# Optimization experiments

Hardware: AMD Instinct MI355X
Metric: run time of the kernel (lower is better)

Reference implementation:

```python
import jax, jax.numpy as jnp
import numpy as np

ALPHA = 2.0
INF = 1e12  # stand-in for +inf, safe in fp32 arithmetic here


def _sq_dt_last(f):
    """Generalized 1D squared distance transform along the last axis.
    D[..., p] = min_q (p - q)^2 + f[..., q]  (Felzenszwalb DT, brute-force min)."""
    n = f.shape[-1]
    i = jnp.arange(n, dtype=f.dtype)
    cost = (i[:, None] - i[None, :]) ** 2  # [q, p]
    # [..., q, 1] + [q, p] -> min over q
    return jnp.min(f[..., :, None] + cost, axis=-2)


def _edt(mask):
    """Exact 2D Euclidean distance transform: distance from each True pixel
    to the nearest False pixel (0 at False pixels), matching scipy's
    distance_transform_edt(mask). mask: bool [B, H, W]."""
    f = jnp.where(mask, jnp.float32(INF), jnp.float32(0.0))
    # pass along H (axis 1)
    f = jnp.moveaxis(_sq_dt_last(jnp.moveaxis(f, 1, -1)), -1, 1)
    # pass along W (axis 2)
    f = _sq_dt_last(f)
    return jnp.sqrt(f)


def _distance_field(img):
    """fg_dist + bg_dist per batch element; zero field if no foreground
    (mirrors the fg_mask.any() check in the torch code)."""
    fg = img > 0.5
    field = _edt(fg) + _edt(~fg)
    has_fg = jnp.any(fg, axis=(1, 2), keepdims=True)
    return jnp.where(has_fg, field, jnp.float32(0.0))


def setup_inputs() -> dict:
    key = jax.random.key(0)
    k1, k2 = jax.random.split(key)
    pred = jax.random.normal(k1, (8, 192, 192), dtype=jnp.float32)   # logits
    target = jax.random.uniform(k2, (8, 192, 192), dtype=jnp.float32)
    return {"pred": pred, "target": target}


def reference(pred, target):
    p = jax.nn.sigmoid(pred)
    # distance fields are computed via numpy/scipy in the original -> constants
    pred_dt = jax.lax.stop_gradient(_distance_field(p))
    target_dt = jax.lax.stop_gradient(_distance_field(target))
    pred_error = (p - target) ** 2
    distance = (pred_dt ** ALPHA + target_dt ** ALPHA) / (pred_dt + target_dt) ** ALPHA
    dt_field = pred_error * distance
    loss = jnp.mean(dt_field, axis=-1)
    return jnp.mean(loss)
```

## Files before the change

kernel.cpp:

```cpp
#include <hip/hip_runtime.h>
#include <stdint.h>

#define B 8
#define H 192
#define W 192
#define NPIX (B * H * W)
#define NROWS (B * H)
#define NCOL (B * W)
#define INFF 1e12f

__device__ __forceinline__ int hi_pos(uint64_t w0, uint64_t w1, uint64_t w2) {
  if (w2) return 191 - __builtin_clzll(w2);
  if (w1) return 127 - __builtin_clzll(w1);
  if (w0) return 63 - __builtin_clzll(w0);
  return -255;
}
__device__ __forceinline__ int lo_pos(uint64_t w0, uint64_t w1, uint64_t w2) {
  if (w0) return __builtin_ctzll(w0);
  if (w1) return 64 + __builtin_ctzll(w1);
  if (w2) return 128 + __builtin_ctzll(w2);
  return 447;
}
__device__ __forceinline__ int nearest_dist(uint64_t s0, uint64_t s1,
                                            uint64_t s2, int h) {
  int k = h >> 6, r = h & 63;
  uint64_t keepL = (2ull << r) - 1;
  uint64_t b0 = s0, b1 = s1, b2 = s2;
  if (k == 0) { b0 &= keepL; b1 = 0; b2 = 0; }
  else if (k == 1) { b1 &= keepL; b2 = 0; }
  else { b2 &= keepL; }
  int dbelow = h - hi_pos(b0, b1, b2);
  uint64_t keepU = (~0ull) << r;
  uint64_t a0 = s0, a1 = s1, a2 = s2;
  if (k == 0) { a0 &= keepU; }
  else if (k == 1) { a0 = 0; a1 &= keepU; }
  else { a0 = 0; a1 = 0; a2 &= keepU; }
  int dabove = lo_pos(a0, a1, a2) - h;
  return min(min(dbelow, dabove), 255);
}

__global__ __launch_bounds__(192) void col_mask(
    const float* __restrict__ pred, const float* __restrict__ targ,
    uint64_t* __restrict__ masks) {
  int bw = blockIdx.x;
  int b = bw / W, w = bw % W;
  int h = threadIdx.x;
  int idx = b * H * W + h * W + w;
  uint64_t bp = __ballot(pred[idx] > 0.0f);
  uint64_t bt = __ballot(targ[idx] > 0.5f);
  if ((h & 63) == 0) {
    int wv = h >> 6;
    masks[wv * NCOL + bw] = bp;
    masks[(3 + wv) * NCOL + bw] = bt;
  }
}

__global__ __launch_bounds__(192) void row_pass(
    const float* __restrict__ pred, const float* __restrict__ targ,
    const uint64_t* __restrict__ masks, float* __restrict__ partial) {
  int bh = blockIdx.x;
  int b = bh / H, h = bh % H;
  int w = threadIdx.x;
  __shared__ uint32_t sm[W];
  __shared__ float wsum[3];
  int cw = b * W + w;
  uint64_t p0 = masks[0 * NCOL + cw], p1 = masks[1 * NCOL + cw],
           p2 = masks[2 * NCOL + cw];
  uint64_t q0 = masks[3 * NCOL + cw], q1 = masks[4 * NCOL + cw],
           q2 = masks[5 * NCOL + cw];
  int base = b * H * W + h * W;
  float xv = pred[base + w];
  float tv = targ[base + w];

  int k = h >> 6, rb = h & 63;
  uint64_t pw = (k == 0) ? p0 : ((k == 1) ? p1 : p2);
  uint64_t qw = (k == 0) ? q0 : ((k == 1) ? q1 : q2);
  int mp = (int)((pw >> rb) & 1);
  int mt = (int)((qw >> rb) & 1);
  int sp = nearest_dist(mp ? ~p0 : p0, mp ? ~p1 : p1, mp ? ~p2 : p2, h);
  int st = nearest_dist(mt ? ~q0 : q0, mt ? ~q1 : q1, mt ? ~q2 : q2, h);
  int dFp = mp ? sp : 0, dTp = mp ? 0 : sp;
  int dFt = mt ? st : 0, dTt = mt ? 0 : st;
  uint32_t own = (uint32_t)dFp | ((uint32_t)dTp << 8) | ((uint32_t)dFt << 16) |
                 ((uint32_t)dTt << 24);
  sm[w] = own;
  __syncthreads();

  int shp = (xv > 0.0f) ? 0 : 8;
  int sht = (tv > 0.5f) ? 16 : 24;
  int dp = (own >> shp) & 255;
  int dt = (own >> sht) & 255;
  float bp = (dp == 255) ? INFF : (float)(dp * dp);
  float bt = (dt == 255) ? INFF : (float)(dt * dt);
  for (int r = 1; r < W; ++r) {
    float rr = (float)(r * r);
    if (rr >= fmaxf(bp, bt)) break;
    int ql = w - r, qr = w + r;
    if (ql >= 0) {
      uint32_t v = sm[ql];
      int a = (v >> shp) & 255, c = (v >> sht) & 255;
      bp = fminf(bp, (a == 255) ? INFF : rr + (float)(a * a));
      bt = fminf(bt, (c == 255) ? INFF : rr + (float)(c * c));
    }
    if (qr < W) {
      uint32_t v = sm[qr];
      int a = (v >> shp) & 255, c = (v >> sht) & 255;
      bp = fminf(bp, (a == 255) ? INFF : rr + (float)(a * a));
      bt = fminf(bt, (c == 255) ? INFF : rr + (float)(c * c));
    }
  }

  float p = 1.0f / (1.0f + __expf(-xv));
  float e = p - tv;
  float err = e * e;
  float pd = sqrtf(bp), td = sqrtf(bt);
  float s = pd + td;
  float term = err * (bp + bt) / (s * s);

  for (int off = 32; off > 0; off >>= 1) term += __shfl_down(term, off, 64);
  if ((w & 63) == 0) wsum[w >> 6] = term;
  __syncthreads();
  if (w == 0) partial[bh] = wsum[0] + wsum[1] + wsum[2];
}

__global__ __launch_bounds__(256) void reduce_pass(
    const float* __restrict__ partial, float* __restrict__ out) {
  int t = threadIdx.x;
  float s = 0.0f;
#pragma unroll
  for (int i = t; i < NROWS; i += 256) s += partial[i];
  for (int off = 32; off > 0; off >>= 1) s += __shfl_down(s, off, 64);
  __shared__ float ws[4];
  if ((t & 63) == 0) ws[t >> 6] = s;
  __syncthreads();
  if (t == 0) out[0] = (ws[0] + ws[1] + ws[2] + ws[3]) * (1.0f / (float)NPIX);
}

extern "C" void kernel_launch(void* const* d_in, const int* in_sizes, int n_in,
                              void* d_out, int out_size, void* d_ws, size_t ws_size,
                              hipStream_t stream) {
  const float* pred = (const float*)d_in[0];
  const float* targ = (const float*)d_in[1];
  float* out = (float*)d_out;
  uint64_t* masks = (uint64_t*)d_ws;
  float* partial = (float*)((char*)d_ws + (size_t)6 * NCOL * 8);

  col_mask<<<NCOL, 192, 0, stream>>>(pred, targ, masks);
  row_pass<<<NROWS, 192, 0, stream>>>(pred, targ, masks, partial);
  reduce_pass<<<1, 256, 0, stream>>>(partial, out);
}
```

Before: 64.87 us.

## Fuse column-mask and row-pass kernels into one block-per-row-group kernel

Merges the column bitmask kernel and the row EDT kernel into one launch. Each block handles one image and a group of 24 rows. The block first builds the column bitmasks for the whole image in shared memory, then processes its rows four at a time with 768 threads. This removes a kernel launch and the global round trip of the masks. In exchange, each of the 8 blocks per image recomputes the full-image masks, which means redundant strided global reads. Only 64 blocks are launched, so occupancy is low.

```diff
diff --git a/kernel.cpp b/kernel.cpp
--- a/kernel.cpp
+++ b/kernel.cpp
@@ -6,8 +6,12 @@
 #define W 192
 #define NPIX (B * H * W)
 #define NROWS (B * H)
-#define NCOL (B * W)
 #define INFF 1e12f
+
+#define SPLITS 8
+#define RPB (H / SPLITS)
+#define SLOTS 4
+#define ITERS (RPB / SLOTS)
 
 __device__ __forceinline__ int hi_pos(uint64_t w0, uint64_t w1, uint64_t w2) {
   if (w2) return 191 - __builtin_clzll(w2);
@@ -39,88 +43,95 @@
   return min(min(dbelow, dabove), 255);
 }
 
-__global__ __launch_bounds__(192) void col_mask(
+__global__ __launch_bounds__(768) void fused_pass(
     const float* __restrict__ pred, const float* __restrict__ targ,
-    uint64_t* __restrict__ masks) {
-  int bw = blockIdx.x;
-  int b = bw / W, w = bw % W;
-  int h = threadIdx.x;
-  int idx = b * H * W + h * W + w;
-  uint64_t bp = __ballot(pred[idx] > 0.0f);
-  uint64_t bt = __ballot(targ[idx] > 0.5f);
-  if ((h & 63) == 0) {
-    int wv = h >> 6;
-    masks[wv * NCOL + bw] = bp;
-    masks[(3 + wv) * NCOL + bw] = bt;
+    float* __restrict__ partial) {
+  int blk = blockIdx.x;
+  int b = blk >> 3, rg = blk & 7;
+  int row0 = rg * RPB;
+  int t = threadIdx.x;
+
+  __shared__ uint64_t cm[2][3][W];
+  __shared__ uint32_t sm[SLOTS][W];
+  __shared__ float wsum[SLOTS][3];
+
+  if (t < 3 * W) {
+    int k = t / W, w = t - k * W;
+    const float* pb = pred + b * H * W;
+    const float* tb = targ + b * H * W;
+    int base = (k << 6) * W + w;
+    uint64_t pw = 0, qw = 0;
+#pragma unroll 16
+    for (int j = 0; j < 64; ++j) {
+      pw |= (uint64_t)(pb[base + j * W] > 0.0f) << j;
+      qw |= (uint64_t)(tb[base + j * W] > 0.5f) << j;
+    }
+    cm[0][k][w] = pw;
+    cm[1][k][w] = qw;
   }
-}
-
-__global__ __launch_bounds__(192) void row_pass(
-    const float* __restrict__ pred, const float* __restrict__ targ,
-    const uint64_t* __restrict__ masks, float* __restrict__ partial) {
-  int bh = blockIdx.x;
-  int b = bh / H, h = bh % H;
-  int w = threadIdx.x;
-  __shared__ uint32_t sm[W];
-  __shared__ float wsum[3];
-  int cw = b * W + w;
-  uint64_t p0 = masks[0 * NCOL + cw], p1 = masks[1 * NCOL + cw],
-           p2 = masks[2 * NCOL + cw];
-  uint64_t q0 = masks[3 * NCOL + cw], q1 = masks[4 * NCOL + cw],
-           q2 = masks[5 * NCOL + cw];
-  int base = b * H * W + h * W;
-  float xv = pred[base + w];
-  float tv = targ[base + w];
-
-  int k = h >> 6, rb = h & 63;
-  uint64_t pw = (k == 0) ? p0 : ((k == 1) ? p1 : p2);
-  uint64_t qw = (k == 0) ? q0 : ((k == 1) ? q1 : q2);
-  int mp = (int)((pw >> rb) & 1);
-  int mt = (int)((qw >> rb) & 1);
-  int sp = nearest_dist(mp ? ~p0 : p0, mp ? ~p1 : p1, mp ? ~p2 : p2, h);
-  int st = nearest_dist(mt ? ~q0 : q0, mt ? ~q1 : q1, mt ? ~q2 : q2, h);
-  int dFp = mp ? sp : 0, dTp = mp ? 0 : sp;
-  int dFt = mt ? st : 0, dTt = mt ? 0 : st;
-  uint32_t own = (uint32_t)dFp | ((uint32_t)dTp << 8) | ((uint32_t)dFt << 16) |
-                 ((uint32_t)dTt << 24);
-  sm[w] = own;
   __syncthreads();
 
-  int shp = (xv > 0.0f) ? 0 : 8;
-  int sht = (tv > 0.5f) ? 16 : 24;
-  int dp = (own >> shp) & 255;
-  int dt = (own >> sht) & 255;
-  float bp = (dp == 255) ? INFF : (float)(dp * dp);
-  float bt = (dt == 255) ? INFF : (float)(dt * dt);
-  for (int r = 1; r < W; ++r) {
-    float rr = (float)(r * r);
-    if (rr >= fmaxf(bp, bt)) break;
-    int ql = w - r, qr = w + r;
-    if (ql >= 0) {
-      uint32_t v = sm[ql];
-      int a = (v >> shp) & 255, c = (v >> sht) & 255;
-      bp = fminf(bp, (a == 255) ? INFF : rr + (float)(a * a));
-      bt = fminf(bt, (c == 255) ? INFF : rr + (float)(c * c));
+  int slot = t / W, w = t - slot * W;
+  uint64_t p0 = cm[0][0][w], p1 = cm[0][1][w], p2 = cm[0][2][w];
+  uint64_t q0 = cm[1][0][w], q1 = cm[1][1][w], q2 = cm[1][2][w];
+
+  for (int it = 0; it < ITERS; ++it) {
+    int h = row0 + it * SLOTS + slot;
+    int base = b * H * W + h * W;
+    float xv = pred[base + w];
+    float tv = targ[base + w];
+
+    int k = h >> 6, rb = h & 63;
+    uint64_t pw = (k == 0) ? p0 : ((k == 1) ? p1 : p2);
+    uint64_t qw = (k == 0) ? q0 : ((k == 1) ? q1 : q2);
+    int mp = (int)((pw >> rb) & 1);
+    int mt = (int)((qw >> rb) & 1);
+    int sp = nearest_dist(mp ? ~p0 : p0, mp ? ~p1 : p1, mp ? ~p2 : p2, h);
+    int st = nearest_dist(mt ? ~q0 : q0, mt ? ~q1 : q1, mt ? ~q2 : q2, h);
+    int dFp = mp ? sp : 0, dTp = mp ? 0 : sp;
+    int dFt = mt ? st : 0, dTt = mt ? 0 : st;
+    uint32_t own = (uint32_t)dFp | ((uint32_t)dTp << 8) |
+                   ((uint32_t)dFt << 16) | ((uint32_t)dTt << 24);
+    sm[slot][w] = own;
+    __syncthreads();
+
+    int shp = (xv > 0.0f) ? 0 : 8;
+    int sht = (tv > 0.5f) ? 16 : 24;
+    int dp = (own >> shp) & 255;
+    int dt = (own >> sht) & 255;
+    float bp = (dp == 255) ? INFF : (float)(dp * dp);
+    float bt = (dt == 255) ? INFF : (float)(dt * dt);
+    for (int r = 1; r < W; ++r) {
+      float rr = (float)(r * r);
+      if (rr >= fmaxf(bp, bt)) break;
+      int ql = w - r, qr = w + r;
+      if (ql >= 0) {
+        uint32_t v = sm[slot][ql];
+        int a = (v >> shp) & 255, c = (v >> sht) & 255;
+        bp = fminf(bp, (a == 255) ? INFF : rr + (float)(a * a));
+        bt = fminf(bt, (c == 255) ? INFF : rr + (float)(c * c));
+      }
+      if (qr < W) {
+        uint32_t v = sm[slot][qr];
+        int a = (v >> shp) & 255, c = (v >> sht) & 255;
+        bp = fminf(bp, (a == 255) ? INFF : rr + (float)(a * a));
+        bt = fminf(bt, (c == 255) ? INFF : rr + (float)(c * c));
+      }
     }
-    if (qr < W) {
-      uint32_t v = sm[qr];
-      int a = (v >> shp) & 255, c = (v >> sht) & 255;
-      bp = fminf(bp, (a == 255) ? INFF : rr + (float)(a * a));
-      bt = fminf(bt, (c == 255) ? INFF : rr + (float)(c * c));
-    }
+
+    float p = 1.0f / (1.0f + __expf(-xv));
+    float e = p - tv;
+    float err = e * e;
+    float pd = sqrtf(bp), td = sqrtf(bt);
+    float s = pd + td;
+    float term = err * (bp + bt) / (s * s);
+
+    for (int off = 32; off > 0; off >>= 1) term += __shfl_down(term, off, 64);
+    if ((w & 63) == 0) wsum[slot][w >> 6] = term;
+    __syncthreads();
+    if (w == 0)
+      partial[b * H + h] = wsum[slot][0] + wsum[slot][1] + wsum[slot][2];
   }
-
-  float p = 1.0f / (1.0f + __expf(-xv));
-  float e = p - tv;
-  float err = e * e;
-  float pd = sqrtf(bp), td = sqrtf(bt);
-  float s = pd + td;
-  float term = err * (bp + bt) / (s * s);
-
-  for (int off = 32; off > 0; off >>= 1) term += __shfl_down(term, off, 64);
-  if ((w & 63) == 0) wsum[w >> 6] = term;
-  __syncthreads();
-  if (w == 0) partial[bh] = wsum[0] + wsum[1] + wsum[2];
 }
 
 __global__ __launch_bounds__(256) void reduce_pass(
@@ -137,15 +148,13 @@
 }
 
 extern "C" void kernel_launch(void* const* d_in, const int* in_sizes, int n_in,
-                              void* d_out, int out_size, void* d_ws, size_t ws_size,
-                              hipStream_t stream) {
+                              void* d_out, int out_size, void* d_ws,
+                              size_t ws_size, hipStream_t stream) {
   const float* pred = (const float*)d_in[0];
   const float* targ = (const float*)d_in[1];
   float* out = (float*)d_out;
-  uint64_t* masks = (uint64_t*)d_ws;
-  float* partial = (float*)((char*)d_ws + (size_t)6 * NCOL * 8);
+  float* partial = (float*)d_ws;
 
-  col_mask<<<NCOL, 192, 0, stream>>>(pred, targ, masks);
-  row_pass<<<NROWS, 192, 0, stream>>>(pred, targ, masks, partial);
+  fused_pass<<<B * SPLITS, 768, 0, stream>>>(pred, targ, partial);
   reduce_pass<<<1, 256, 0, stream>>>(partial, out);
 }
```

Measured after the change: 75.42 us. 1.16x slower.

## Process four rows per block and fold final reduction into atomics

Applied to the files above, without the earlier changes.

The row pass now handles four image rows per block (two slots of 192 threads, two iterations), so each thread loads the six column mask words once and reuses them for several rows. The separate reduction kernel is removed. Each block atomically adds its scaled partial sum into the output, which is zeroed in the column-mask kernel. This drops one kernel launch and reuses mask loads, at the cost of fewer, larger blocks, more barriers per block, and float atomics that make the summation order nondeterministic.

```diff
diff --git a/kernel.cpp b/kernel.cpp
--- a/kernel.cpp
+++ b/kernel.cpp
@@ -8,6 +8,12 @@
 #define NROWS (B * H)
 #define NCOL (B * W)
 #define INFF 1e12f
+
+#define SLOTS 2
+#define ITERS 2
+#define ROWS_PB (SLOTS * ITERS)
+#define NTHR (SLOTS * W)
+#define KBLK (NROWS / ROWS_PB)
 
 __device__ __forceinline__ int hi_pos(uint64_t w0, uint64_t w1, uint64_t w2) {
   if (w2) return 191 - __builtin_clzll(w2);
@@ -41,7 +47,7 @@
 
 __global__ __launch_bounds__(192) void col_mask(
     const float* __restrict__ pred, const float* __restrict__ targ,
-    uint64_t* __restrict__ masks) {
+    uint64_t* __restrict__ masks, float* __restrict__ out) {
   int bw = blockIdx.x;
   int b = bw / W, w = bw % W;
   int h = threadIdx.x;
@@ -53,99 +59,100 @@
     masks[wv * NCOL + bw] = bp;
     masks[(3 + wv) * NCOL + bw] = bt;
   }
+  if (bw == 0 && h == 0) out[0] = 0.0f;
 }
 
-__global__ __launch_bounds__(192) void row_pass(
+__global__ __launch_bounds__(NTHR) void row_pass(
     const float* __restrict__ pred, const float* __restrict__ targ,
-    const uint64_t* __restrict__ masks, float* __restrict__ partial) {
-  int bh = blockIdx.x;
-  int b = bh / H, h = bh % H;
-  int w = threadIdx.x;
-  __shared__ uint32_t sm[W];
-  __shared__ float wsum[3];
+    const uint64_t* __restrict__ masks, float* __restrict__ out) {
+  int blk = blockIdx.x;
+  int bh0 = blk * ROWS_PB;
+  int b = bh0 / H, h0 = bh0 - b * H;
+  int t = threadIdx.x;
+  int slot = t / W, w = t - slot * W;
+
+  __shared__ uint32_t sm[SLOTS][W];
+  __shared__ float wsum[SLOTS][3];
+  __shared__ float rsum[ROWS_PB];
+
   int cw = b * W + w;
   uint64_t p0 = masks[0 * NCOL + cw], p1 = masks[1 * NCOL + cw],
            p2 = masks[2 * NCOL + cw];
   uint64_t q0 = masks[3 * NCOL + cw], q1 = masks[4 * NCOL + cw],
            q2 = masks[5 * NCOL + cw];
-  int base = b * H * W + h * W;
-  float xv = pred[base + w];
-  float tv = targ[base + w];
 
-  int k = h >> 6, rb = h & 63;
-  uint64_t pw = (k == 0) ? p0 : ((k == 1) ? p1 : p2);
-  uint64_t qw = (k == 0) ? q0 : ((k == 1) ? q1 : q2);
-  int mp = (int)((pw >> rb) & 1);
-  int mt = (int)((qw >> rb) & 1);
-  int sp = nearest_dist(mp ? ~p0 : p0, mp ? ~p1 : p1, mp ? ~p2 : p2, h);
-  int st = nearest_dist(mt ? ~q0 : q0, mt ? ~q1 : q1, mt ? ~q2 : q2, h);
-  int dFp = mp ? sp : 0, dTp = mp ? 0 : sp;
-  int dFt = mt ? st : 0, dTt = mt ? 0 : st;
-  uint32_t own = (uint32_t)dFp | ((uint32_t)dTp << 8) | ((uint32_t)dFt << 16) |
-                 ((uint32_t)dTt << 24);
-  sm[w] = own;
+  for (int it = 0; it < ITERS; ++it) {
+    int h = h0 + it * SLOTS + slot;
+    int base = b * H * W + h * W;
+    float xv = pred[base + w];
+    float tv = targ[base + w];
+
+    int k = h >> 6, rb = h & 63;
+    uint64_t pw = (k == 0) ? p0 : ((k == 1) ? p1 : p2);
+    uint64_t qw = (k == 0) ? q0 : ((k == 1) ? q1 : q2);
+    int mp = (int)((pw >> rb) & 1);
+    int mt = (int)((qw >> rb) & 1);
+    int sp = nearest_dist(mp ? ~p0 : p0, mp ? ~p1 : p1, mp ? ~p2 : p2, h);
+    int st = nearest_dist(mt ? ~q0 : q0, mt ? ~q1 : q1, mt ? ~q2 : q2, h);
+    int dFp = mp ? sp : 0, dTp = mp ? 0 : sp;
+    int dFt = mt ? st : 0, dTt = mt ? 0 : st;
+    uint32_t own = (uint32_t)dFp | ((uint32_t)dTp << 8) |
+                   ((uint32_t)dFt << 16) | ((uint32_t)dTt << 24);
+    sm[slot][w] = own;
+    __syncthreads();
+
+    int shp = (xv > 0.0f) ? 0 : 8;
+    int sht = (tv > 0.5f) ? 16 : 24;
+    int dp = (own >> shp) & 255;
+    int dt = (own >> sht) & 255;
+    float bp = (dp == 255) ? INFF : (float)(dp * dp);
+    float bt = (dt == 255) ? INFF : (float)(dt * dt);
+    for (int r = 1; r < W; ++r) {
+      float rr = (float)(r * r);
+      if (rr >= fmaxf(bp, bt)) break;
+      int ql = w - r, qr = w + r;
+      if (ql >= 0) {
+        uint32_t v = sm[slot][ql];
+        int a = (v >> shp) & 255, c = (v >> sht) & 255;
+        bp = fminf(bp, (a == 255) ? INFF : rr + (float)(a * a));
+        bt = fminf(bt, (c == 255) ? INFF : rr + (float)(c * c));
+      }
+      if (qr < W) {
+        uint32_t v = sm[slot][qr];
+        int a = (v >> shp) & 255, c = (v >> sht) & 255;
+        bp = fminf(bp, (a == 255) ? INFF : rr + (float)(a * a));
+        bt = fminf(bt, (c == 255) ? INFF : rr + (float)(c * c));
+      }
+    }
+
+    float p = 1.0f / (1.0f + __expf(-xv));
+    float e = p - tv;
+    float err = e * e;
+    float pd = sqrtf(bp), td = sqrtf(bt);
+    float s = pd + td;
+    float term = err * (bp + bt) / (s * s);
+
+    for (int off = 32; off > 0; off >>= 1) term += __shfl_down(term, off, 64);
+    if ((w & 63) == 0) wsum[slot][w >> 6] = term;
+    __syncthreads();
+    if (w == 0)
+      rsum[it * SLOTS + slot] = wsum[slot][0] + wsum[slot][1] + wsum[slot][2];
+  }
   __syncthreads();
-
-  int shp = (xv > 0.0f) ? 0 : 8;
-  int sht = (tv > 0.5f) ? 16 : 24;
-  int dp = (own >> shp) & 255;
-  int dt = (own >> sht) & 255;
-  float bp = (dp == 255) ? INFF : (float)(dp * dp);
-  float bt = (dt == 255) ? INFF : (float)(dt * dt);
-  for (int r = 1; r < W; ++r) {
-    float rr = (float)(r * r);
-    if (rr >= fmaxf(bp, bt)) break;
-    int ql = w - r, qr = w + r;
-    if (ql >= 0) {
-      uint32_t v = sm[ql];
-      int a = (v >> shp) & 255, c = (v >> sht) & 255;
-      bp = fminf(bp, (a == 255) ? INFF : rr + (float)(a * a));
-      bt = fminf(bt, (c == 255) ? INFF : rr + (float)(c * c));
-    }
-    if (qr < W) {
-      uint32_t v = sm[qr];
-      int a = (v >> shp) & 255, c = (v >> sht) & 255;
-      bp = fminf(bp, (a == 255) ? INFF : rr + (float)(a * a));
-      bt = fminf(bt, (c == 255) ? INFF : rr + (float)(c * c));
-    }
+  if (t == 0) {
+    float bsum = (rsum[0] + rsum[1]) + (rsum[2] + rsum[3]);
+    atomicAdd(out, bsum * (1.0f / (float)NPIX));
   }
-
-  float p = 1.0f / (1.0f + __expf(-xv));
-  float e = p - tv;
-  float err = e * e;
-  float pd = sqrtf(bp), td = sqrtf(bt);
-  float s = pd + td;
-  float term = err * (bp + bt) / (s * s);
-
-  for (int off = 32; off > 0; off >>= 1) term += __shfl_down(term, off, 64);
-  if ((w & 63) == 0) wsum[w >> 6] = term;
-  __syncthreads();
-  if (w == 0) partial[bh] = wsum[0] + wsum[1] + wsum[2];
-}
-
-__global__ __launch_bounds__(256) void reduce_pass(
-    const float* __restrict__ partial, float* __restrict__ out) {
-  int t = threadIdx.x;
-  float s = 0.0f;
-#pragma unroll
-  for (int i = t; i < NROWS; i += 256) s += partial[i];
-  for (int off = 32; off > 0; off >>= 1) s += __shfl_down(s, off, 64);
-  __shared__ float ws[4];
-  if ((t & 63) == 0) ws[t >> 6] = s;
-  __syncthreads();
-  if (t == 0) out[0] = (ws[0] + ws[1] + ws[2] + ws[3]) * (1.0f / (float)NPIX);
 }
 
 extern "C" void kernel_launch(void* const* d_in, const int* in_sizes, int n_in,
-                              void* d_out, int out_size, void* d_ws, size_t ws_size,
-                              hipStream_t stream) {
+                              void* d_out, int out_size, void* d_ws,
+                              size_t ws_size, hipStream_t stream) {
   const float* pred = (const float*)d_in[0];
   const float* targ = (const float*)d_in[1];
   float* out = (float*)d_out;
   uint64_t* masks = (uint64_t*)d_ws;
-  float* partial = (float*)((char*)d_ws + (size_t)6 * NCOL * 8);
 
-  col_mask<<<NCOL, 192, 0, stream>>>(pred, targ, masks);
-  row_pass<<<NROWS, 192, 0, stream>>>(pred, targ, masks, partial);
-  reduce_pass<<<1, 256, 0, stream>>>(partial, out);
+  col_mask<<<NCOL, 192, 0, stream>>>(pred, targ, masks, out);
+  row_pass<<<KBLK, NTHR, 0, stream>>>(pred, targ, masks, out);
 }
```

New measurement: 67.51 us. 4.1% more time.

## Build column bitmasks from coalesced row tiles with shared-memory bit transpose

Applied to the files above, without the earlier changes.

The column-mask kernel used to read one column per block with strided loads (one float per row, stride W). It now loads 64x64 tiles with lanes reading contiguous row segments, ballots each row into a 64-bit row mask in shared memory, then transposes the bits so each thread builds one column word. This replaces poorly coalesced global reads with coalesced ones, at the cost of far fewer blocks (72 versus 1536) and a serial 64-iteration bit-gather loop per output thread.

```diff
diff --git a/kernel.cpp b/kernel.cpp
--- a/kernel.cpp
+++ b/kernel.cpp
@@ -39,19 +39,47 @@
   return min(min(dbelow, dabove), 255);
 }
 
-__global__ __launch_bounds__(192) void col_mask(
+__global__ __launch_bounds__(256) void col_mask(
     const float* __restrict__ pred, const float* __restrict__ targ,
     uint64_t* __restrict__ masks) {
-  int bw = blockIdx.x;
-  int b = bw / W, w = bw % W;
-  int h = threadIdx.x;
-  int idx = b * H * W + h * W + w;
-  uint64_t bp = __ballot(pred[idx] > 0.0f);
-  uint64_t bt = __ballot(targ[idx] > 0.5f);
-  if ((h & 63) == 0) {
-    int wv = h >> 6;
-    masks[wv * NCOL + bw] = bp;
-    masks[(3 + wv) * NCOL + bw] = bt;
+  int blk = blockIdx.x;
+  int b = blk / 9;
+  int rem = blk - b * 9;
+  int wg = rem / 3, k = rem - wg * 3;
+  int t = threadIdx.x;
+  int lane = t & 63, wv = t >> 6;
+
+  __shared__ uint64_t rmp[64];
+  __shared__ uint64_t rmt[64];
+
+  {
+    int j0 = wv * 16;
+    int base = b * H * W + (k * 64 + j0) * W + wg * 64 + lane;
+    float pv[16], tv[16];
+#pragma unroll
+    for (int jj = 0; jj < 16; ++jj) {
+      pv[jj] = pred[base + jj * W];
+      tv[jj] = targ[base + jj * W];
+    }
+#pragma unroll
+    for (int jj = 0; jj < 16; ++jj) {
+      uint64_t bp = __ballot(pv[jj] > 0.0f);
+      uint64_t bt = __ballot(tv[jj] > 0.5f);
+      if (lane == 0) {
+        rmp[j0 + jj] = bp;
+        rmt[j0 + jj] = bt;
+      }
+    }
+  }
+  __syncthreads();
+
+  if (t < 128) {
+    const uint64_t* rm = (t >= 64) ? rmt : rmp;
+    uint64_t wrd = 0;
+#pragma unroll
+    for (int j = 0; j < 64; ++j) wrd |= ((rm[j] >> lane) & 1ull) << j;
+    int word_row = ((t >= 64) ? 3 : 0) + k;
+    masks[word_row * NCOL + b * W + wg * 64 + lane] = wrd;
   }
 }
 
@@ -137,15 +165,15 @@
 }
 
 extern "C" void kernel_launch(void* const* d_in, const int* in_sizes, int n_in,
-                              void* d_out, int out_size, void* d_ws, size_t ws_size,
-                              hipStream_t stream) {
+                              void* d_out, int out_size, void* d_ws,
+                              size_t ws_size, hipStream_t stream) {
   const float* pred = (const float*)d_in[0];
   const float* targ = (const float*)d_in[1];
   float* out = (float*)d_out;
   uint64_t* masks = (uint64_t*)d_ws;
   float* partial = (float*)((char*)d_ws + (size_t)6 * NCOL * 8);
 
-  col_mask<<<NCOL, 192, 0, stream>>>(pred, targ, masks);
+  col_mask<<<B * 3 * 3, 256, 0, stream>>>(pred, targ, masks);
   row_pass<<<NROWS, 192, 0, stream>>>(pred, targ, masks, partial);
   reduce_pass<<<1, 256, 0, stream>>>(partial, out);
 }
```

Result: no change. 64.85 us (-0.0%).
